# Kernel tuning notes

Hardware: AMD Instinct MI355X
Metric: run time of the kernel (lower is better)

The kernel has to match this reference:

```python
import jax, jax.numpy as jnp
import numpy as np

N_NODES = 50000
EMBED_DIM = 512
N_EDGES = 800000
NEG_SLOPE = 0.01  # nn.LeakyReLU default


def setup_inputs() -> dict:
    key = jax.random.key(0)
    k1, k2, k3 = jax.random.split(key, 3)
    X = jax.random.normal(k1, (N_NODES, EMBED_DIM), dtype=jnp.float32)
    # Glorot-ish scale for the GCNConv weight
    W = jax.random.normal(k2, (EMBED_DIM, EMBED_DIM), dtype=jnp.float32) / np.sqrt(EMBED_DIM)
    b = jnp.zeros((EMBED_DIM,), dtype=jnp.float32)
    edge_index = jax.random.randint(k3, (2, N_EDGES), 0, N_NODES, dtype=jnp.int32)
    return {"X": X, "W": W, "b": b, "edge_index": edge_index}


def reference(X, W, b, edge_index):
    N = X.shape[0]
    # GCNConv: add self-loops, symmetric normalization deg^-1/2 A deg^-1/2
    loop = jnp.arange(N, dtype=edge_index.dtype)
    src = jnp.concatenate([edge_index[0], loop])  # [E+N]
    dst = jnp.concatenate([edge_index[1], loop])  # [E+N]
    deg = jax.ops.segment_sum(jnp.ones_like(dst, dtype=X.dtype), dst, num_segments=N)
    dinv = jnp.where(deg > 0, jax.lax.rsqrt(deg), 0.0)  # deg^{-1/2}, inf->0
    norm = dinv[src] * dinv[dst]                         # [E+N]
    H = X @ W                                            # [N, D] dense GEMM
    msgs = H[src] * norm[:, None]                        # [E+N, D] gathered messages
    out = jax.ops.segment_sum(msgs, dst, num_segments=N) + b
    # LeakyReLU activation; Dropout is identity in eval mode
    return jnp.where(out >= 0, out, NEG_SLOPE * out)
```

## Files before the change

kernel.cpp:

```cpp
#include <hip/hip_runtime.h>
#include <cstdint>
#include <cstddef>

#define DFEAT 512
#define BM 128
#define BN 128
#define BK 32

typedef __attribute__((ext_vector_type(8))) short bf16x8;
typedef __attribute__((ext_vector_type(4))) float f32x4;

#define GLOBAL_AS __attribute__((address_space(1)))
#define LDS_AS __attribute__((address_space(3)))

__device__ __forceinline__ unsigned short f2bf(float f) {
  unsigned u = __float_as_uint(f);
  u = u + 0x7fffu + ((u >> 16) & 1u);
  return (unsigned short)(u >> 16);
}

__device__ __forceinline__ float bf2f_lo(unsigned u) { return __uint_as_float(u << 16); }
__device__ __forceinline__ float bf2f_hi(unsigned u) { return __uint_as_float(u & 0xffff0000u); }

__device__ __forceinline__ void gl_lds16(const void* g, void* l) {
  __builtin_amdgcn_global_load_lds((const GLOBAL_AS unsigned int*)g,
                                   (LDS_AS unsigned int*)l, 16, 0, 0);
}

__global__ void k_init(int* __restrict__ deg, int* __restrict__ fill, int N) {
  int i = blockIdx.x * blockDim.x + threadIdx.x;
  if (i < N) { deg[i] = 1; fill[i] = 0; }
}

__global__ void k_count(const int* __restrict__ dst, int* __restrict__ deg, int E) {
  int i = blockIdx.x * blockDim.x + threadIdx.x;
  if (i < E) atomicAdd(&deg[dst[i]], 1);
}

__global__ void k_dinv(const int* __restrict__ deg, float* __restrict__ dinv, int N) {
  int i = blockIdx.x * blockDim.x + threadIdx.x;
  if (i < N) dinv[i] = rsqrtf((float)deg[i]);
}

__global__ void k_scan(const int* __restrict__ deg, int* __restrict__ rowStart, int N) {
  const int t = threadIdx.x;
  const int C = (N + 1023) / 1024;
  int lo = t * C;
  int hi = lo + C; if (hi > N) hi = N; if (lo > N) lo = N;
  int sum = 0;
  for (int i = lo; i < hi; ++i) sum += deg[i];
  __shared__ int sm[1024];
  sm[t] = sum;
  __syncthreads();
  for (int d = 1; d < 1024; d <<= 1) {
    int v = (t >= d) ? sm[t - d] : 0;
    __syncthreads();
    sm[t] += v;
    __syncthreads();
  }
  int off = sm[t] - sum;
  for (int i = lo; i < hi; ++i) { rowStart[i] = off; off += deg[i]; }
  if (t == 1023) rowStart[N] = sm[1023];
}

__global__ void k_fill(const int* __restrict__ src, const int* __restrict__ dst,
                       const int* __restrict__ rowStart, int* __restrict__ fill,
                       int2* __restrict__ cw, const float* __restrict__ dinv, int E, int N) {
  int i = blockIdx.x * blockDim.x + threadIdx.x;
  if (i >= E + N) return;
  int d, s;
  if (i < E) { d = dst[i]; s = src[i]; }
  else       { d = i - E; s = d; }
  int pos = rowStart[d] + atomicAdd(&fill[d], 1);
  int2 q; q.x = s; q.y = __float_as_int(dinv[s]);
  cw[pos] = q;
}

__global__ void k_wt(const float* __restrict__ W, unsigned short* __restrict__ Wt) {
  int i = blockIdx.x * blockDim.x + threadIdx.x;
  int k = i >> 9, n = i & 511;
  Wt[(size_t)n * DFEAT + k] = f2bf(W[i]);
}

__global__ void k_xb(const float* __restrict__ X, unsigned short* __restrict__ Xb, int total8) {
  int i = blockIdx.x * blockDim.x + threadIdx.x;
  if (i >= total8) return;
  const float4 a = *reinterpret_cast<const float4*>(X + (size_t)i * 8);
  const float4 c = *reinterpret_cast<const float4*>(X + (size_t)i * 8 + 4);
  uint4 o;
  o.x = (unsigned)f2bf(a.x) | ((unsigned)f2bf(a.y) << 16);
  o.y = (unsigned)f2bf(a.z) | ((unsigned)f2bf(a.w) << 16);
  o.z = (unsigned)f2bf(c.x) | ((unsigned)f2bf(c.y) << 16);
  o.w = (unsigned)f2bf(c.z) | ((unsigned)f2bf(c.w) << 16);
  *reinterpret_cast<uint4*>(Xb + (size_t)i * 8) = o;
}

template <bool TAIL>
__device__ __forceinline__ void agg8(const unsigned short* __restrict__ Xb,
                                     const int2* __restrict__ cw,
                                     int p, int e, int lane, float* acc) {
  int2 q[8];
#pragma unroll
  for (int i = 0; i < 8; ++i) {
    int pi = p + i;
    if (TAIL) pi = (pi < e) ? pi : (e - 1);
    q[i] = cw[pi];
  }
  uint4 v[8];
#pragma unroll
  for (int i = 0; i < 8; ++i)
    v[i] = *reinterpret_cast<const uint4*>(Xb + (size_t)q[i].x * DFEAT + lane * 8);
#pragma unroll
  for (int i = 0; i < 8; ++i) {
    float w = __int_as_float(q[i].y);
    if (TAIL) w = (p + i < e) ? w : 0.0f;
    acc[0] = fmaf(w, bf2f_lo(v[i].x), acc[0]); acc[1] = fmaf(w, bf2f_hi(v[i].x), acc[1]);
    acc[2] = fmaf(w, bf2f_lo(v[i].y), acc[2]); acc[3] = fmaf(w, bf2f_hi(v[i].y), acc[3]);
    acc[4] = fmaf(w, bf2f_lo(v[i].z), acc[4]); acc[5] = fmaf(w, bf2f_hi(v[i].z), acc[5]);
    acc[6] = fmaf(w, bf2f_lo(v[i].w), acc[6]); acc[7] = fmaf(w, bf2f_hi(v[i].w), acc[7]);
  }
}

__global__ __launch_bounds__(256) void k_aggregate(const unsigned short* __restrict__ Xb,
                                                   const int2* __restrict__ cw,
                                                   const int* __restrict__ rowStart,
                                                   const float* __restrict__ dinv,
                                                   unsigned short* __restrict__ Y, int N) {
  const int row = blockIdx.x * 4 + (threadIdx.x >> 6);
  const int lane = threadIdx.x & 63;
  float acc[8] = {0.f, 0.f, 0.f, 0.f, 0.f, 0.f, 0.f, 0.f};
  if (row < N) {
    const int s = rowStart[row], e = rowStart[row + 1];
    int p = s;
    for (; p + 8 <= e; p += 8) agg8<false>(Xb, cw, p, e, lane, acc);
    if (p < e) agg8<true>(Xb, cw, p, e, lane, acc);
    const float sc = dinv[row];
#pragma unroll
    for (int j = 0; j < 8; ++j) acc[j] *= sc;
  }
  uint4 o;
  o.x = (unsigned)f2bf(acc[0]) | ((unsigned)f2bf(acc[1]) << 16);
  o.y = (unsigned)f2bf(acc[2]) | ((unsigned)f2bf(acc[3]) << 16);
  o.z = (unsigned)f2bf(acc[4]) | ((unsigned)f2bf(acc[5]) << 16);
  o.w = (unsigned)f2bf(acc[6]) | ((unsigned)f2bf(acc[7]) << 16);
  *reinterpret_cast<uint4*>(Y + (size_t)row * DFEAT + lane * 8) = o;
}

__global__ __launch_bounds__(256) void k_gemm(const unsigned short* __restrict__ Y,
                                              const unsigned short* __restrict__ Wt,
                                              const float* __restrict__ bias,
                                              float* __restrict__ out, int M) {
  __shared__ unsigned short As[BM * BK];
  __shared__ unsigned short Bs[BN * BK];
  const int tid = threadIdx.x;
  const int lane = tid & 63;
  const int wave = tid >> 6;
  const int l16 = lane & 15;
  const int quad = lane >> 4;
  const int wm = (wave >> 1) * 64;
  const int wn = (wave & 1) * 64;

  const int nwg = gridDim.x;
  const int q8 = nwg >> 3, r8 = nwg & 7;
  const int xcd = blockIdx.x & 7, loc = blockIdx.x >> 3;
  const int wg = (xcd < r8 ? xcd * (q8 + 1) : r8 * (q8 + 1) + (xcd - r8) * q8) + loc;
  const int m0 = (wg >> 2) * BM;
  const int n0 = (wg & 3) * BN;

  f32x4 acc[4][4];
#pragma unroll
  for (int mi = 0; mi < 4; ++mi)
#pragma unroll
    for (int ni = 0; ni < 4; ++ni) { f32x4 z = {0.f, 0.f, 0.f, 0.f}; acc[mi][ni] = z; }

  const int ci0 = wave * 64 + lane;
  const int ci1 = 256 + ci0;
  const int ra0 = ci0 >> 2, ka0 = (((ci0 & 3) - (ra0 >> 1)) & 3) * 8;
  const int ra1 = ci1 >> 2, ka1 = (((ci1 & 3) - (ra1 >> 1)) & 3) * 8;

  const unsigned short* Ag0 = Y + (size_t)(m0 + ra0) * DFEAT + ka0;
  const unsigned short* Ag1 = Y + (size_t)(m0 + ra1) * DFEAT + ka1;
  const unsigned short* Bg0 = Wt + (size_t)(n0 + ra0) * DFEAT + ka0;
  const unsigned short* Bg1 = Wt + (size_t)(n0 + ra1) * DFEAT + ka1;
  unsigned short* La0 = As + ci0 * 8;
  unsigned short* La1 = As + ci1 * 8;
  unsigned short* Lb0 = Bs + ci0 * 8;
  unsigned short* Lb1 = Bs + ci1 * 8;

  const int rotA = (quad + ((wm + l16) >> 1)) & 3;
  const int rotB = (quad + ((wn + l16) >> 1)) & 3;
  const unsigned short* AsRd = As + (wm + l16) * BK + rotA * 8;
  const unsigned short* BsRd = Bs + (wn + l16) * BK + rotB * 8;

  for (int kk = 0; kk < DFEAT; kk += BK) {
    gl_lds16(Ag0 + kk, La0);
    gl_lds16(Ag1 + kk, La1);
    gl_lds16(Bg0 + kk, Lb0);
    gl_lds16(Bg1 + kk, Lb1);
    __syncthreads();
    bf16x8 av[4], bv[4];
#pragma unroll
    for (int mi = 0; mi < 4; ++mi)
      av[mi] = *reinterpret_cast<const bf16x8*>(AsRd + mi * 16 * BK);
#pragma unroll
    for (int ni = 0; ni < 4; ++ni)
      bv[ni] = *reinterpret_cast<const bf16x8*>(BsRd + ni * 16 * BK);
#pragma unroll
    for (int mi = 0; mi < 4; ++mi)
#pragma unroll
      for (int ni = 0; ni < 4; ++ni)
        acc[mi][ni] = __builtin_amdgcn_mfma_f32_16x16x32_bf16(av[mi], bv[ni], acc[mi][ni], 0, 0, 0);
    __syncthreads();
  }

  float bvals[4];
#pragma unroll
  for (int ni = 0; ni < 4; ++ni) bvals[ni] = bias[n0 + wn + 16 * ni + l16];

#pragma unroll
  for (int mi = 0; mi < 4; ++mi) {
#pragma unroll
    for (int r = 0; r < 4; ++r) {
      int row = m0 + wm + 16 * mi + quad * 4 + r;
      if (row < M) {
#pragma unroll
        for (int ni = 0; ni < 4; ++ni) {
          float v = acc[mi][ni][r] + bvals[ni];
          v = (v >= 0.f) ? v : 0.01f * v;
          out[(size_t)row * DFEAT + n0 + wn + 16 * ni + l16] = v;
        }
      }
    }
  }
}

extern "C" void kernel_launch(void* const* d_in, const int* in_sizes, int n_in,
                              void* d_out, int out_size, void* d_ws, size_t ws_size,
                              hipStream_t stream) {
  const float* X = (const float*)d_in[0];
  const float* W = (const float*)d_in[1];
  const float* b = (const float*)d_in[2];
  const int* ei  = (const int*)d_in[3];
  const int D = DFEAT;
  const int N = in_sizes[0] / D;
  const int E = in_sizes[3] / 2;
  const int* src = ei;
  const int* dst = ei + E;
  float* out = (float*)d_out;

  uintptr_t p = (uintptr_t)d_ws;
  auto carve = [&](size_t bytes) -> void* {
    uintptr_t r = p;
    p += (bytes + 255) & ~(size_t)255;
    return (void*)r;
  };
  int*   deg      = (int*)carve(sizeof(int) * (size_t)N);
  int*   fill     = (int*)carve(sizeof(int) * (size_t)N);
  int*   rowStart = (int*)carve(sizeof(int) * (size_t)(N + 1));
  float* dinv     = (float*)carve(sizeof(float) * (size_t)N);
  int2*  cw       = (int2*)carve(sizeof(int2) * (size_t)(E + N));
  unsigned short* Wt = (unsigned short*)carve(sizeof(unsigned short) * (size_t)D * D);
  const int Mtiles = (N + BM - 1) / BM;
  const int Mpad = Mtiles * BM;
  unsigned short* Y  = (unsigned short*)carve(sizeof(unsigned short) * (size_t)Mpad * D);

  unsigned short* Xb = (unsigned short*)d_out;

  hipLaunchKernelGGL(k_init,  dim3((N + 255) / 256), dim3(256), 0, stream, deg, fill, N);
  hipLaunchKernelGGL(k_count, dim3((E + 255) / 256), dim3(256), 0, stream, dst, deg, E);
  hipLaunchKernelGGL(k_dinv,  dim3((N + 255) / 256), dim3(256), 0, stream, deg, dinv, N);
  hipLaunchKernelGGL(k_scan,  dim3(1), dim3(1024), 0, stream, deg, rowStart, N);
  hipLaunchKernelGGL(k_fill,  dim3((E + N + 255) / 256), dim3(256), 0, stream,
                     src, dst, rowStart, fill, cw, dinv, E, N);
  hipLaunchKernelGGL(k_wt,    dim3((D * D) / 256), dim3(256), 0, stream, W, Wt);
  hipLaunchKernelGGL(k_xb,    dim3((N * D / 8 + 255) / 256), dim3(256), 0, stream,
                     X, Xb, N * D / 8);
  hipLaunchKernelGGL(k_aggregate, dim3(Mpad / 4), dim3(256), 0, stream,
                     Xb, cw, rowStart, dinv, Y, N);
  hipLaunchKernelGGL(k_gemm,  dim3(Mtiles * 4), dim3(256), 0, stream, Y, Wt, b, out, N);
}
```

Measured before the change: 501.4 us.

## Split aggregation into XCD-mapped feature slabs and fuse small prep kernels

The aggregation kernel is restructured so each block handles one 32-wide feature slab across 32 rows. Blocks are mapped so that each XCD works on one slab per pass, which keeps the gathered slice of Xb for that slab within the XCD's L2. Edge records are read with nontemporal loads and Y is written with nontemporal stores. Separately, the dinv kernel is removed (rsqrt is computed inline from deg) and the W-transpose and X-convert kernels are merged into one launch. The trade-offs are 8-byte gathers per lane instead of 16-byte ones, 16 passes over the edge list, and lanes within a wave idling up to the maximum degree of the 8 rows they share.

```diff
diff --git a/kernel.cpp b/kernel.cpp
--- a/kernel.cpp
+++ b/kernel.cpp
@@ -7,6 +7,11 @@
 #define BN 128
 #define BK 32
 
+#define SLABW 32
+#define NSLAB (DFEAT / SLABW)
+#define RPW 8
+#define RPB 32
+
 typedef __attribute__((ext_vector_type(8))) short bf16x8;
 typedef __attribute__((ext_vector_type(4))) float f32x4;
 
@@ -35,11 +40,6 @@
 __global__ void k_count(const int* __restrict__ dst, int* __restrict__ deg, int E) {
   int i = blockIdx.x * blockDim.x + threadIdx.x;
   if (i < E) atomicAdd(&deg[dst[i]], 1);
-}
-
-__global__ void k_dinv(const int* __restrict__ deg, float* __restrict__ dinv, int N) {
-  int i = blockIdx.x * blockDim.x + threadIdx.x;
-  if (i < N) dinv[i] = rsqrtf((float)deg[i]);
 }
 
 __global__ void k_scan(const int* __restrict__ deg, int* __restrict__ rowStart, int N) {
@@ -65,25 +65,27 @@
 
 __global__ void k_fill(const int* __restrict__ src, const int* __restrict__ dst,
                        const int* __restrict__ rowStart, int* __restrict__ fill,
-                       int2* __restrict__ cw, const float* __restrict__ dinv, int E, int N) {
+                       int2* __restrict__ cw, const int* __restrict__ deg, int E, int N) {
   int i = blockIdx.x * blockDim.x + threadIdx.x;
   if (i >= E + N) return;
   int d, s;
   if (i < E) { d = dst[i]; s = src[i]; }
   else       { d = i - E; s = d; }
   int pos = rowStart[d] + atomicAdd(&fill[d], 1);
-  int2 q; q.x = s; q.y = __float_as_int(dinv[s]);
+  int2 q; q.x = s; q.y = __float_as_int(rsqrtf((float)deg[s]));
   cw[pos] = q;
 }
 
-__global__ void k_wt(const float* __restrict__ W, unsigned short* __restrict__ Wt) {
-  int i = blockIdx.x * blockDim.x + threadIdx.x;
-  int k = i >> 9, n = i & 511;
-  Wt[(size_t)n * DFEAT + k] = f2bf(W[i]);
-}
-
-__global__ void k_xb(const float* __restrict__ X, unsigned short* __restrict__ Xb, int total8) {
-  int i = blockIdx.x * blockDim.x + threadIdx.x;
+__global__ void k_wtxb(const float* __restrict__ W, unsigned short* __restrict__ Wt,
+                       const float* __restrict__ X, unsigned short* __restrict__ Xb,
+                       int total8) {
+  if (blockIdx.x < 1024) {
+    int i = blockIdx.x * 256 + threadIdx.x;
+    int k = i >> 9, n = i & 511;
+    Wt[(size_t)n * DFEAT + k] = f2bf(W[i]);
+    return;
+  }
+  int i = (blockIdx.x - 1024) * 256 + threadIdx.x;
   if (i >= total8) return;
   const float4 a = *reinterpret_cast<const float4*>(X + (size_t)i * 8);
   const float4 c = *reinterpret_cast<const float4*>(X + (size_t)i * 8 + 4);
@@ -95,55 +97,65 @@
   *reinterpret_cast<uint4*>(Xb + (size_t)i * 8) = o;
 }
 
-template <bool TAIL>
-__device__ __forceinline__ void agg8(const unsigned short* __restrict__ Xb,
-                                     const int2* __restrict__ cw,
-                                     int p, int e, int lane, float* acc) {
-  int2 q[8];
-#pragma unroll
-  for (int i = 0; i < 8; ++i) {
-    int pi = p + i;
-    if (TAIL) pi = (pi < e) ? pi : (e - 1);
-    q[i] = cw[pi];
-  }
-  uint4 v[8];
-#pragma unroll
-  for (int i = 0; i < 8; ++i)
-    v[i] = *reinterpret_cast<const uint4*>(Xb + (size_t)q[i].x * DFEAT + lane * 8);
-#pragma unroll
-  for (int i = 0; i < 8; ++i) {
-    float w = __int_as_float(q[i].y);
-    if (TAIL) w = (p + i < e) ? w : 0.0f;
-    acc[0] = fmaf(w, bf2f_lo(v[i].x), acc[0]); acc[1] = fmaf(w, bf2f_hi(v[i].x), acc[1]);
-    acc[2] = fmaf(w, bf2f_lo(v[i].y), acc[2]); acc[3] = fmaf(w, bf2f_hi(v[i].y), acc[3]);
-    acc[4] = fmaf(w, bf2f_lo(v[i].z), acc[4]); acc[5] = fmaf(w, bf2f_hi(v[i].z), acc[5]);
-    acc[6] = fmaf(w, bf2f_lo(v[i].w), acc[6]); acc[7] = fmaf(w, bf2f_hi(v[i].w), acc[7]);
-  }
-}
-
 __global__ __launch_bounds__(256) void k_aggregate(const unsigned short* __restrict__ Xb,
                                                    const int2* __restrict__ cw,
                                                    const int* __restrict__ rowStart,
-                                                   const float* __restrict__ dinv,
-                                                   unsigned short* __restrict__ Y, int N) {
-  const int row = blockIdx.x * 4 + (threadIdx.x >> 6);
+                                                   unsigned short* __restrict__ Y,
+                                                   int N, int RB) {
+  const int xcd = blockIdx.x & 7;
+  const int ord = blockIdx.x >> 3;
+  const int pass = (ord >= RB) ? 1 : 0;
+  const int rb = ord - pass * RB;
+  const int slab = xcd + 8 * pass;
+  const int wave = threadIdx.x >> 6;
   const int lane = threadIdx.x & 63;
-  float acc[8] = {0.f, 0.f, 0.f, 0.f, 0.f, 0.f, 0.f, 0.f};
-  if (row < N) {
-    const int s = rowStart[row], e = rowStart[row + 1];
-    int p = s;
-    for (; p + 8 <= e; p += 8) agg8<false>(Xb, cw, p, e, lane, acc);
-    if (p < e) agg8<true>(Xb, cw, p, e, lane, acc);
-    const float sc = dinv[row];
-#pragma unroll
-    for (int j = 0; j < 8; ++j) acc[j] *= sc;
-  }
-  uint4 o;
-  o.x = (unsigned)f2bf(acc[0]) | ((unsigned)f2bf(acc[1]) << 16);
-  o.y = (unsigned)f2bf(acc[2]) | ((unsigned)f2bf(acc[3]) << 16);
-  o.z = (unsigned)f2bf(acc[4]) | ((unsigned)f2bf(acc[5]) << 16);
-  o.w = (unsigned)f2bf(acc[6]) | ((unsigned)f2bf(acc[7]) << 16);
-  *reinterpret_cast<uint4*>(Y + (size_t)row * DFEAT + lane * 8) = o;
+  const int r = lane >> 3;
+  const int f = lane & 7;
+  const int row = rb * RPB + wave * RPW + r;
+
+  int s = 0, deg = 0;
+  if (row < N) { s = rowStart[row]; deg = rowStart[row + 1] - s; }
+
+  int md = deg;
+  { int t_ = __shfl_xor(md, 8);  md = md > t_ ? md : t_; }
+  { int t_ = __shfl_xor(md, 16); md = md > t_ ? md : t_; }
+  { int t_ = __shfl_xor(md, 32); md = md > t_ ? md : t_; }
+
+  const unsigned short* xs = Xb + (size_t)slab * SLABW + (size_t)f * 4;
+  float a0 = 0.f, a1 = 0.f, a2 = 0.f, a3 = 0.f;
+
+  for (int t = 0; t < md; t += 4) {
+    unsigned long long q[4];
+#pragma unroll
+    for (int i = 0; i < 4; ++i) {
+      int tt = t + i;
+      int pi = (tt < deg) ? s + tt : s;
+      q[i] = __builtin_nontemporal_load(
+          reinterpret_cast<const unsigned long long*>(cw + pi));
+    }
+    uint2 v[4];
+#pragma unroll
+    for (int i = 0; i < 4; ++i) {
+      const int sx = (int)(unsigned)q[i];
+      v[i] = *reinterpret_cast<const uint2*>(xs + (size_t)sx * DFEAT);
+    }
+#pragma unroll
+    for (int i = 0; i < 4; ++i) {
+      const float w = (t + i < deg) ? __uint_as_float((unsigned)(q[i] >> 32)) : 0.f;
+      a0 = fmaf(w, bf2f_lo(v[i].x), a0);
+      a1 = fmaf(w, bf2f_hi(v[i].x), a1);
+      a2 = fmaf(w, bf2f_lo(v[i].y), a2);
+      a3 = fmaf(w, bf2f_hi(v[i].y), a3);
+    }
+  }
+  if (deg > 0) {
+    const float sc = rsqrtf((float)deg);
+    a0 *= sc; a1 *= sc; a2 *= sc; a3 *= sc;
+  }
+  unsigned long long o = (unsigned long long)((unsigned)f2bf(a0) | ((unsigned)f2bf(a1) << 16))
+                       | ((unsigned long long)((unsigned)f2bf(a2) | ((unsigned)f2bf(a3) << 16)) << 32);
+  __builtin_nontemporal_store(o,
+      reinterpret_cast<unsigned long long*>(Y + (size_t)row * DFEAT + slab * SLABW + f * 4));
 }
 
 __global__ __launch_bounds__(256) void k_gemm(const unsigned short* __restrict__ Y,
@@ -257,7 +269,6 @@
   int*   deg      = (int*)carve(sizeof(int) * (size_t)N);
   int*   fill     = (int*)carve(sizeof(int) * (size_t)N);
   int*   rowStart = (int*)carve(sizeof(int) * (size_t)(N + 1));
-  float* dinv     = (float*)carve(sizeof(float) * (size_t)N);
   int2*  cw       = (int2*)carve(sizeof(int2) * (size_t)(E + N));
   unsigned short* Wt = (unsigned short*)carve(sizeof(unsigned short) * (size_t)D * D);
   const int Mtiles = (N + BM - 1) / BM;
@@ -266,16 +277,17 @@
 
   unsigned short* Xb = (unsigned short*)d_out;
 
+  const int total8 = N * D / 8;
+  const int RB = Mpad / RPB;
+
   hipLaunchKernelGGL(k_init,  dim3((N + 255) / 256), dim3(256), 0, stream, deg, fill, N);
   hipLaunchKernelGGL(k_count, dim3((E + 255) / 256), dim3(256), 0, stream, dst, deg, E);
-  hipLaunchKernelGGL(k_dinv,  dim3((N + 255) / 256), dim3(256), 0, stream, deg, dinv, N);
   hipLaunchKernelGGL(k_scan,  dim3(1), dim3(1024), 0, stream, deg, rowStart, N);
   hipLaunchKernelGGL(k_fill,  dim3((E + N + 255) / 256), dim3(256), 0, stream,
-                     src, dst, rowStart, fill, cw, dinv, E, N);
-  hipLaunchKernelGGL(k_wt,    dim3((D * D) / 256), dim3(256), 0, stream, W, Wt);
-  hipLaunchKernelGGL(k_xb,    dim3((N * D / 8 + 255) / 256), dim3(256), 0, stream,
-                     X, Xb, N * D / 8);
-  hipLaunchKernelGGL(k_aggregate, dim3(Mpad / 4), dim3(256), 0, stream,
-                     Xb, cw, rowStart, dinv, Y, N);
+                     src, dst, rowStart, fill, cw, deg, E, N);
+  hipLaunchKernelGGL(k_wtxb,  dim3(1024 + (total8 + 255) / 256), dim3(256), 0, stream,
+                     W, Wt, X, Xb, total8);
+  hipLaunchKernelGGL(k_aggregate, dim3(16 * RB), dim3(256), 0, stream,
+                     Xb, cw, rowStart, Y, N, RB);
   hipLaunchKernelGGL(k_gemm,  dim3(Mtiles * 4), dim3(256), 0, stream, Y, Wt, b, out, N);
 }
```

After: 725.3 us. +44.7%, slower.

## Fuse preprocessing kernels, drop dinv/fill arrays, split aggregation into four launches

Applied to the files above, without the earlier changes.

Merges the degree count, W transpose and X-to-bf16 conversion into a single launch, and replaces the init kernel with a memset. The dinv array is removed: degrees are recomputed with rsqrt from deg inside the fill and aggregate kernels. The scan now writes a fill-position array directly, so the fill kernel needs only one atomic per edge and no extra rowStart read. The aggregation is split into four launches over row quarters, which adds launch overhead and has no obvious speed benefit.

```diff
diff --git a/kernel.cpp b/kernel.cpp
--- a/kernel.cpp
+++ b/kernel.cpp
@@ -27,63 +27,26 @@
                                    (LDS_AS unsigned int*)l, 16, 0, 0);
 }
 
-__global__ void k_init(int* __restrict__ deg, int* __restrict__ fill, int N) {
-  int i = blockIdx.x * blockDim.x + threadIdx.x;
-  if (i < N) { deg[i] = 1; fill[i] = 0; }
-}
-
-__global__ void k_count(const int* __restrict__ dst, int* __restrict__ deg, int E) {
-  int i = blockIdx.x * blockDim.x + threadIdx.x;
-  if (i < E) atomicAdd(&deg[dst[i]], 1);
-}
-
-__global__ void k_dinv(const int* __restrict__ deg, float* __restrict__ dinv, int N) {
-  int i = blockIdx.x * blockDim.x + threadIdx.x;
-  if (i < N) dinv[i] = rsqrtf((float)deg[i]);
-}
-
-__global__ void k_scan(const int* __restrict__ deg, int* __restrict__ rowStart, int N) {
-  const int t = threadIdx.x;
-  const int C = (N + 1023) / 1024;
-  int lo = t * C;
-  int hi = lo + C; if (hi > N) hi = N; if (lo > N) lo = N;
-  int sum = 0;
-  for (int i = lo; i < hi; ++i) sum += deg[i];
-  __shared__ int sm[1024];
-  sm[t] = sum;
-  __syncthreads();
-  for (int d = 1; d < 1024; d <<= 1) {
-    int v = (t >= d) ? sm[t - d] : 0;
-    __syncthreads();
-    sm[t] += v;
-    __syncthreads();
-  }
-  int off = sm[t] - sum;
-  for (int i = lo; i < hi; ++i) { rowStart[i] = off; off += deg[i]; }
-  if (t == 1023) rowStart[N] = sm[1023];
-}
-
-__global__ void k_fill(const int* __restrict__ src, const int* __restrict__ dst,
-                       const int* __restrict__ rowStart, int* __restrict__ fill,
-                       int2* __restrict__ cw, const float* __restrict__ dinv, int E, int N) {
-  int i = blockIdx.x * blockDim.x + threadIdx.x;
-  if (i >= E + N) return;
-  int d, s;
-  if (i < E) { d = dst[i]; s = src[i]; }
-  else       { d = i - E; s = d; }
-  int pos = rowStart[d] + atomicAdd(&fill[d], 1);
-  int2 q; q.x = s; q.y = __float_as_int(dinv[s]);
-  cw[pos] = q;
-}
-
-__global__ void k_wt(const float* __restrict__ W, unsigned short* __restrict__ Wt) {
-  int i = blockIdx.x * blockDim.x + threadIdx.x;
-  int k = i >> 9, n = i & 511;
-  Wt[(size_t)n * DFEAT + k] = f2bf(W[i]);
-}
-
-__global__ void k_xb(const float* __restrict__ X, unsigned short* __restrict__ Xb, int total8) {
-  int i = blockIdx.x * blockDim.x + threadIdx.x;
+__global__ void k_pre(const int* __restrict__ dst, int* __restrict__ deg, int E,
+                      const float* __restrict__ W, unsigned short* __restrict__ Wt,
+                      const float* __restrict__ X, unsigned short* __restrict__ Xb,
+                      int total8) {
+  const int cb = (E + 255) >> 8;
+  int b = blockIdx.x;
+  if (b < cb) {
+    int i = b * 256 + threadIdx.x;
+    if (i < E) atomicAdd(&deg[dst[i]], 1);
+    return;
+  }
+  b -= cb;
+  if (b < 1024) {
+    int i = b * 256 + threadIdx.x;
+    int k = i >> 9, n = i & 511;
+    Wt[(size_t)n * DFEAT + k] = f2bf(W[i]);
+    return;
+  }
+  b -= 1024;
+  int i = b * 256 + threadIdx.x;
   if (i >= total8) return;
   const float4 a = *reinterpret_cast<const float4*>(X + (size_t)i * 8);
   const float4 c = *reinterpret_cast<const float4*>(X + (size_t)i * 8 + 4);
@@ -95,6 +58,45 @@
   *reinterpret_cast<uint4*>(Xb + (size_t)i * 8) = o;
 }
 
+__global__ __launch_bounds__(1024) void k_scan(const int* __restrict__ deg,
+                                               int* __restrict__ rowStart,
+                                               int* __restrict__ fillPos, int N) {
+  const int t = threadIdx.x;
+  const int C = (N + 1023) / 1024;
+  int lo = t * C;
+  int hi = lo + C; if (hi > N) hi = N; if (lo > N) lo = N;
+  int sum = 0;
+  for (int i = lo; i < hi; ++i) sum += deg[i] + 1;
+  __shared__ int sm[1024];
+  sm[t] = sum;
+  __syncthreads();
+  for (int d = 1; d < 1024; d <<= 1) {
+    int v = (t >= d) ? sm[t - d] : 0;
+    __syncthreads();
+    sm[t] += v;
+    __syncthreads();
+  }
+  int off = sm[t] - sum;
+  for (int i = lo; i < hi; ++i) {
+    rowStart[i] = off; fillPos[i] = off;
+    off += deg[i] + 1;
+  }
+  if (t == 1023) rowStart[N] = sm[1023];
+}
+
+__global__ void k_fill(const int* __restrict__ src, const int* __restrict__ dst,
+                       int* __restrict__ fillPos, int2* __restrict__ cw,
+                       const int* __restrict__ deg, int E, int N) {
+  int i = blockIdx.x * blockDim.x + threadIdx.x;
+  if (i >= E + N) return;
+  int d, s;
+  if (i < E) { d = dst[i]; s = src[i]; }
+  else       { d = i - E; s = d; }
+  int pos = atomicAdd(&fillPos[d], 1);
+  int2 q; q.x = s; q.y = __float_as_int(rsqrtf((float)(deg[s] + 1)));
+  cw[pos] = q;
+}
+
 template <bool TAIL>
 __device__ __forceinline__ void agg8(const unsigned short* __restrict__ Xb,
                                      const int2* __restrict__ cw,
@@ -124,9 +126,9 @@
 __global__ __launch_bounds__(256) void k_aggregate(const unsigned short* __restrict__ Xb,
                                                    const int2* __restrict__ cw,
                                                    const int* __restrict__ rowStart,
-                                                   const float* __restrict__ dinv,
-                                                   unsigned short* __restrict__ Y, int N) {
-  const int row = blockIdx.x * 4 + (threadIdx.x >> 6);
+                                                   unsigned short* __restrict__ Y,
+                                                   int N, int rowOff) {
+  const int row = rowOff + blockIdx.x * 4 + (threadIdx.x >> 6);
   const int lane = threadIdx.x & 63;
   float acc[8] = {0.f, 0.f, 0.f, 0.f, 0.f, 0.f, 0.f, 0.f};
   if (row < N) {
@@ -134,7 +136,7 @@
     int p = s;
     for (; p + 8 <= e; p += 8) agg8<false>(Xb, cw, p, e, lane, acc);
     if (p < e) agg8<true>(Xb, cw, p, e, lane, acc);
-    const float sc = dinv[row];
+    const float sc = rsqrtf((float)(e - s));
 #pragma unroll
     for (int j = 0; j < 8; ++j) acc[j] *= sc;
   }
@@ -255,9 +257,8 @@
     return (void*)r;
   };
   int*   deg      = (int*)carve(sizeof(int) * (size_t)N);
-  int*   fill     = (int*)carve(sizeof(int) * (size_t)N);
   int*   rowStart = (int*)carve(sizeof(int) * (size_t)(N + 1));
-  float* dinv     = (float*)carve(sizeof(float) * (size_t)N);
+  int*   fillPos  = (int*)carve(sizeof(int) * (size_t)N);
   int2*  cw       = (int2*)carve(sizeof(int2) * (size_t)(E + N));
   unsigned short* Wt = (unsigned short*)carve(sizeof(unsigned short) * (size_t)D * D);
   const int Mtiles = (N + BM - 1) / BM;
@@ -266,16 +267,22 @@
 
   unsigned short* Xb = (unsigned short*)d_out;
 
-  hipLaunchKernelGGL(k_init,  dim3((N + 255) / 256), dim3(256), 0, stream, deg, fill, N);
-  hipLaunchKernelGGL(k_count, dim3((E + 255) / 256), dim3(256), 0, stream, dst, deg, E);
-  hipLaunchKernelGGL(k_dinv,  dim3((N + 255) / 256), dim3(256), 0, stream, deg, dinv, N);
-  hipLaunchKernelGGL(k_scan,  dim3(1), dim3(1024), 0, stream, deg, rowStart, N);
+  const int total8 = N * D / 8;
+  const int cb = (E + 255) / 256;
+  const int xb = (total8 + 255) / 256;
+  const int quarter = ((Mpad / 4 + 3) & ~3);
+
+  hipMemsetAsync(deg, 0, sizeof(int) * (size_t)N, stream);
+  hipLaunchKernelGGL(k_pre,   dim3(cb + 1024 + xb), dim3(256), 0, stream,
+                     dst, deg, E, W, Wt, X, Xb, total8);
+  hipLaunchKernelGGL(k_scan,  dim3(1), dim3(1024), 0, stream, deg, rowStart, fillPos, N);
   hipLaunchKernelGGL(k_fill,  dim3((E + N + 255) / 256), dim3(256), 0, stream,
-                     src, dst, rowStart, fill, cw, dinv, E, N);
-  hipLaunchKernelGGL(k_wt,    dim3((D * D) / 256), dim3(256), 0, stream, W, Wt);
-  hipLaunchKernelGGL(k_xb,    dim3((N * D / 8 + 255) / 256), dim3(256), 0, stream,
-                     X, Xb, N * D / 8);
-  hipLaunchKernelGGL(k_aggregate, dim3(Mpad / 4), dim3(256), 0, stream,
-                     Xb, cw, rowStart, dinv, Y, N);
+                     src, dst, fillPos, cw, deg, E, N);
+  for (int qq = 0; qq < 4; ++qq) {
+    const int ro = qq * quarter;
+    const int nr = (qq == 3) ? (Mpad - 3 * quarter) : quarter;
+    hipLaunchKernelGGL(k_aggregate, dim3(nr / 4), dim3(256), 0, stream,
+                       Xb, cw, rowStart, Y, N, ro);
+  }
   hipLaunchKernelGGL(k_gemm,  dim3(Mtiles * 4), dim3(256), 0, stream, Y, Wt, b, out, N);
 }
```

After: 534.0 us. +6.5%, slower.
